# Performance work log

Hardware: AMD Instinct MI355X
Metric: run time of the kernel (lower is better)

## Reference

```python
import jax, jax.numpy as jnp
import numpy as np

FRAME_NUMBER = 16
FRAME_SIZE = 128
SAMPLE_NUM = 16
NUM_EVENTS = 1048576


def setup_inputs() -> dict:
    key = jax.random.key(0)
    k1, k2, k3, k4 = jax.random.split(key, 4)
    event_values = jax.random.normal(k1, (SAMPLE_NUM, NUM_EVENTS), dtype=jnp.float32)
    # indices rows: (t, x, y). t sorted ascending so torch's `indices[0, -1] + 1`
    # sizing logic is valid; x, y in [0, FRAME_SIZE).
    t_idx = jnp.sort(jax.random.randint(k2, (NUM_EVENTS,), 0, NUM_EVENTS // FRAME_NUMBER, dtype=jnp.int64))
    x_idx = jax.random.randint(k3, (NUM_EVENTS,), 0, FRAME_SIZE, dtype=jnp.int64)
    y_idx = jax.random.randint(k4, (NUM_EVENTS,), 0, FRAME_SIZE, dtype=jnp.int64)
    idx0 = jnp.stack([t_idx, x_idx, y_idx], axis=0)  # [3, num_events]
    # Module only reads event_indices[0]; replicate across samples for shape fidelity.
    event_indices = jnp.broadcast_to(idx0[None], (SAMPLE_NUM, 3, NUM_EVENTS))
    return {"event_values": event_values, "event_indices": event_indices, "use_soft": 0}


def reference(event_values, event_indices, use_soft):
    # Hard split by number (use_soft=False path).
    # coalesce over (t,x,y) + sparse.sum over t == scatter-add over (x,y) per window.
    S, N = event_values.shape
    F, FS = FRAME_NUMBER, FRAME_SIZE
    W = N // F  # time_window (events per frame)

    x_idx = event_indices[0, 1]  # [N], shared across samples (module uses indices[0])
    y_idx = event_indices[0, 2]  # [N]
    frame_id = jnp.arange(N, dtype=x_idx.dtype) // W  # which frame each event falls in
    seg = (frame_id * FS + x_idx) * FS + y_idx  # flat (frame, x, y) bin id, [N]

    pos = jax.nn.relu(event_values)   # [S, N]
    neg = jax.nn.relu(-event_values)  # [S, N]

    num_segments = F * FS * FS
    # segment_sum over events -> [F*FS*FS, S], then reshape to [F, X, Y, S]
    pos_f = jax.ops.segment_sum(pos.T, seg, num_segments=num_segments).reshape(F, FS, FS, S)
    neg_f = jax.ops.segment_sum(neg.T, seg, num_segments=num_segments).reshape(F, FS, FS, S)

    frames = jnp.stack([neg_f, pos_f], axis=1)  # [F, 2, X, Y, S]
    # torch: permute(-1,0,1,3,2) -> [S,F,2,Y,X], then transpose(0,1) -> [F,S,2,Y,X]
    return jnp.transpose(frames, (0, 4, 1, 3, 2))
```

## Files before the change

kernel.cpp:

```cpp
#include <hip/hip_runtime.h>

#define SAMPLES 16
#define NEVENTS (1 << 20)
#define FRAMES  16
#define FSZ     128
#define WIN     (NEVENTS / FRAMES)
#define BINS    (FSZ * FSZ)
#define TPB     1024

__global__ __launch_bounds__(TPB) void frame_accum_kernel(
    const float* __restrict__ ev,
    const int*   __restrict__ idx,
    float*       __restrict__ out)
{
    extern __shared__ float lds[];
    const int tid = threadIdx.x;
    const int s = blockIdx.x & (SAMPLES - 1);
    const int f = blockIdx.x >> 4;

    float4* lds4 = (float4*)lds;
#pragma unroll
    for (int i = 0; i < (2 * BINS / 4) / TPB; ++i)
        lds4[i * TPB + tid] = make_float4(0.f, 0.f, 0.f, 0.f);
    __syncthreads();

    const float* evp = ev  + (size_t)s * NEVENTS     + (size_t)f * WIN;
    const int*   xp  = idx + (size_t)NEVENTS         + (size_t)f * WIN;
    const int*   yp  = idx + (size_t)2 * NEVENTS     + (size_t)f * WIN;

#pragma unroll 4
    for (int i = 0; i < WIN / (4 * TPB); ++i) {
        const int e = (i * TPB + tid) * 4;
        const float4 v  = *(const float4*)(evp + e);
        const int4   xv = *(const int4*)(xp + e);
        const int4   yv = *(const int4*)(yp + e);
        const int px = (int)(((__float_as_uint(v.x) >> 31) ^ 1u) << 14);
        const int py = (int)(((__float_as_uint(v.y) >> 31) ^ 1u) << 14);
        const int pz = (int)(((__float_as_uint(v.z) >> 31) ^ 1u) << 14);
        const int pw = (int)(((__float_as_uint(v.w) >> 31) ^ 1u) << 14);
        atomicAdd(&lds[px + yv.x * FSZ + xv.x], fabsf(v.x));
        atomicAdd(&lds[py + yv.y * FSZ + xv.y], fabsf(v.y));
        atomicAdd(&lds[pz + yv.z * FSZ + xv.z], fabsf(v.z));
        atomicAdd(&lds[pw + yv.w * FSZ + xv.w], fabsf(v.w));
    }
    __syncthreads();

    float4* op = (float4*)(out + ((size_t)(f * SAMPLES + s)) * 2 * BINS);
#pragma unroll
    for (int i = 0; i < (2 * BINS / 4) / TPB; ++i)
        op[i * TPB + tid] = lds4[i * TPB + tid];
}

extern "C" void kernel_launch(void* const* d_in, const int* in_sizes, int n_in,
                              void* d_out, int out_size, void* d_ws, size_t ws_size,
                              hipStream_t stream) {
    const float* ev  = (const float*)d_in[0];
    const int*   idx = (const int*)d_in[1];
    float* out = (float*)d_out;

    (void)hipFuncSetAttribute((const void*)frame_accum_kernel,
                              hipFuncAttributeMaxDynamicSharedMemorySize,
                              2 * BINS * (int)sizeof(float));

    frame_accum_kernel<<<FRAMES * SAMPLES, TPB, 2 * BINS * sizeof(float), stream>>>(
        ev, idx, out);
}
```

Before: 335.7 us.

## Double-buffer event loads ahead of LDS atomics and use nontemporal streaming

Restructures the per-block event loop into an explicit two-stage software pipeline: loads for the next 8-events-per-thread step are issued before the LDS atomics for the current step run, so global memory latency is hidden behind atomic work. Event values are read with nontemporal loads and the output is written with nontemporal stores to avoid polluting cache with single-use data. The change raises register pressure at 1024 threads per block, which could limit occupancy or cause spills.

```diff
diff --git a/kernel.cpp b/kernel.cpp
--- a/kernel.cpp
+++ b/kernel.cpp
@@ -7,6 +7,31 @@
 #define WIN     (NEVENTS / FRAMES)
 #define BINS    (FSZ * FSZ)
 #define TPB     1024
+#define EPT     8
+#define STEPS   (WIN / (EPT * TPB))
+
+typedef float v4f __attribute__((ext_vector_type(4)));
+typedef int   v4i __attribute__((ext_vector_type(4)));
+
+
+__device__ __forceinline__ void acc4(float* lds, v4f v, v4i xv, v4i yv) {
+    const int px = (int)(((__float_as_uint(v.x) >> 31) ^ 1u) << 14);
+    const int py = (int)(((__float_as_uint(v.y) >> 31) ^ 1u) << 14);
+    const int pz = (int)(((__float_as_uint(v.z) >> 31) ^ 1u) << 14);
+    const int pw = (int)(((__float_as_uint(v.w) >> 31) ^ 1u) << 14);
+    atomicAdd(&lds[px + yv.x * FSZ + xv.x], fabsf(v.x));
+    atomicAdd(&lds[py + yv.y * FSZ + xv.y], fabsf(v.y));
+    atomicAdd(&lds[pz + yv.z * FSZ + xv.z], fabsf(v.z));
+    atomicAdd(&lds[pw + yv.w * FSZ + xv.w], fabsf(v.w));
+}
+
+#define LOAD(B, step)                                                          \
+    v##B##a = __builtin_nontemporal_load(&ev4[(step) * 2 * TPB + tid]);        \
+    v##B##b = __builtin_nontemporal_load(&ev4[(step) * 2 * TPB + TPB + tid]);  \
+    x##B##a = x4[(step) * 2 * TPB + tid];                                      \
+    x##B##b = x4[(step) * 2 * TPB + TPB + tid];                                \
+    y##B##a = y4[(step) * 2 * TPB + tid];                                      \
+    y##B##b = y4[(step) * 2 * TPB + TPB + tid];
 
 __global__ __launch_bounds__(TPB) void frame_accum_kernel(
     const float* __restrict__ ev,
@@ -18,37 +43,36 @@
     const int s = blockIdx.x & (SAMPLES - 1);
     const int f = blockIdx.x >> 4;
 
-    float4* lds4 = (float4*)lds;
+    v4f* lds4 = (v4f*)lds;
+    const v4f zero4 = (v4f)(0.f);
 #pragma unroll
     for (int i = 0; i < (2 * BINS / 4) / TPB; ++i)
-        lds4[i * TPB + tid] = make_float4(0.f, 0.f, 0.f, 0.f);
+        lds4[i * TPB + tid] = zero4;
     __syncthreads();
 
-    const float* evp = ev  + (size_t)s * NEVENTS     + (size_t)f * WIN;
-    const int*   xp  = idx + (size_t)NEVENTS         + (size_t)f * WIN;
-    const int*   yp  = idx + (size_t)2 * NEVENTS     + (size_t)f * WIN;
+    const v4f* ev4 = (const v4f*)(ev  + (size_t)s * NEVENTS + (size_t)f * WIN);
+    const v4i* x4  = (const v4i*)(idx + (size_t)NEVENTS      + (size_t)f * WIN);
+    const v4i* y4  = (const v4i*)(idx + (size_t)2 * NEVENTS  + (size_t)f * WIN);
 
-#pragma unroll 4
-    for (int i = 0; i < WIN / (4 * TPB); ++i) {
-        const int e = (i * TPB + tid) * 4;
-        const float4 v  = *(const float4*)(evp + e);
-        const int4   xv = *(const int4*)(xp + e);
-        const int4   yv = *(const int4*)(yp + e);
-        const int px = (int)(((__float_as_uint(v.x) >> 31) ^ 1u) << 14);
-        const int py = (int)(((__float_as_uint(v.y) >> 31) ^ 1u) << 14);
-        const int pz = (int)(((__float_as_uint(v.z) >> 31) ^ 1u) << 14);
-        const int pw = (int)(((__float_as_uint(v.w) >> 31) ^ 1u) << 14);
-        atomicAdd(&lds[px + yv.x * FSZ + xv.x], fabsf(v.x));
-        atomicAdd(&lds[py + yv.y * FSZ + xv.y], fabsf(v.y));
-        atomicAdd(&lds[pz + yv.z * FSZ + xv.z], fabsf(v.z));
-        atomicAdd(&lds[pw + yv.w * FSZ + xv.w], fabsf(v.w));
+    v4f vAa, vAb, vBa, vBb;
+    v4i xAa, xAb, xBa, xBb, yAa, yAb, yBa, yBb;
+
+    LOAD(A, 0)
+#pragma unroll
+    for (int st = 0; st < STEPS; st += 2) {
+        LOAD(B, st + 1)
+        acc4(lds, vAa, xAa, yAa);
+        acc4(lds, vAb, xAb, yAb);
+        if (st + 2 < STEPS) { LOAD(A, st + 2) }
+        acc4(lds, vBa, xBa, yBa);
+        acc4(lds, vBb, xBb, yBb);
     }
     __syncthreads();
 
-    float4* op = (float4*)(out + ((size_t)(f * SAMPLES + s)) * 2 * BINS);
+    v4f* op4 = (v4f*)(out + ((size_t)(f * SAMPLES + s)) * 2 * BINS);
 #pragma unroll
     for (int i = 0; i < (2 * BINS / 4) / TPB; ++i)
-        op[i * TPB + tid] = lds4[i * TPB + tid];
+        __builtin_nontemporal_store(lds4[i * TPB + tid], &op4[i * TPB + tid]);
 }
 
 extern "C" void kernel_launch(void* const* d_in, const int* in_sizes, int n_in,
```

Measured after the change: 342.5 us. 2.0% more time.
